# Kernel optimization log

Measured on AMD Instinct MI355X. Metric: run time of the kernel, lower is better.

Reference implementation:

```python
import jax, jax.numpy as jnp
import numpy as np

D = 512          # latent_dim
H = 8            # num_heads
NLAYERS = 8
DFF = 8          # fast_transformers d_ff slot receives num_heads in the repo (kept faithful)
NC = 10          # NUM_CLUSTERS
KMEANS_ITERS = 10
NJ, NF, T, BS = 25, 6, 1024, 16
NCLS, MAXA = 12, 6


def _pe(S, d):
    pos = jnp.arange(S, dtype=jnp.float32)[:, None]
    div = jnp.exp(jnp.arange(0, d, 2, dtype=jnp.float32) * (-np.log(10000.0) / d))
    pe = jnp.zeros((S, d), jnp.float32)
    pe = pe.at[:, 0::2].set(jnp.sin(pos * div))
    pe = pe.at[:, 1::2].set(jnp.cos(pos * div))
    return pe


def _ln(x, g, b, eps=1e-5):
    m = jnp.mean(x, -1, keepdims=True)
    v = jnp.var(x, -1, keepdims=True)
    return (x - m) * jax.lax.rsqrt(v + eps) * g + b


def _clustered_attn_one(q, k, v):
    # q, k, v: (L, Dh). Cluster queries (Lloyd k-means, deterministic init from
    # first NC queries), attend with centroids, broadcast back to queries.
    cent = q[:NC]
    for _ in range(KMEANS_ITERS):
        d = jnp.sum(cent * cent, -1)[None, :] - 2.0 * (q @ cent.T)  # (L, C)
        a = jnp.argmin(d, -1)
        oh = jax.nn.one_hot(a, NC, dtype=q.dtype)                   # (L, C)
        cent = (oh.T @ q) / jnp.maximum(oh.sum(0), 1.0)[:, None]
    d = jnp.sum(cent * cent, -1)[None, :] - 2.0 * (q @ cent.T)
    a = jnp.argmin(d, -1)                                           # (L,)
    temp = 1.0 / np.sqrt(q.shape[-1])
    A = jax.nn.softmax((cent @ k.T) * temp, -1)                     # (C, L)
    return (A @ v)[a]                                               # (L, Dh)


def _layer(z, Wq, bq, Wk, bk, Wv, bv, Wo, bo, g1, c1, g2, c2, W1, b1, W2, b2):
    B, S, d = z.shape
    Dh = d // H
    q = (z @ Wq + bq).reshape(B, S, H, Dh).transpose(0, 2, 1, 3).reshape(B * H, S, Dh)
    k = (z @ Wk + bk).reshape(B, S, H, Dh).transpose(0, 2, 1, 3).reshape(B * H, S, Dh)
    v = (z @ Wv + bv).reshape(B, S, H, Dh).transpose(0, 2, 1, 3).reshape(B * H, S, Dh)
    o = jax.vmap(_clustered_attn_one)(q, k, v)
    o = o.reshape(B, H, S, Dh).transpose(0, 2, 1, 3).reshape(B, S, d)
    z = z + (o @ Wo + bo)                     # post-norm TransformerEncoderLayer
    z = _ln(z, g1, c1)
    y = jax.nn.relu(z @ W1 + b1) @ W2 + b2    # d_ff == num_heads (repo bug, kept)
    return _ln(z + y, g2, c2)


def _forward(x, muQuery, sigmaQuery, mu_w, mu_b, sig_w, sig_b, skel_w, skel_b,
             Wq, bq, Wk, bk, Wv, bv, Wo, bo, g1, c1, g2, c2, W1, b1, W2, b2, y):
    bs, nj, nf, nframes = x.shape
    h = x.transpose(3, 0, 1, 2).reshape(nframes, bs, nj * nf) @ skel_w + skel_b  # (T,B,D)
    mu_enc = muQuery[y].reshape(bs, -1) @ mu_w + mu_b          # (B, D)
    sig_enc = sigmaQuery[y].reshape(bs, -1) @ sig_w + sig_b    # (B, D)
    xseq = jnp.concatenate([mu_enc[None], sig_enc[None], h], 0)  # (S, B, D)
    S = xseq.shape[0]
    xseq = xseq + _pe(S, xseq.shape[-1])[:, None, :]
    z = xseq.transpose(1, 0, 2)  # (B, S, D): attend over the sequence axis
    for i in range(NLAYERS):
        z = _layer(z, Wq[i], bq[i], Wk[i], bk[i], Wv[i], bv[i], Wo[i], bo[i],
                   g1[i], c1[i], g2[i], c2[i], W1[i], b1[i], W2[i], b2[i])
    out = z.transpose(1, 0, 2)  # (S, B, D)
    return out[0], out[1]       # mu, logvar: (B, D) each


def setup_inputs() -> dict:
    key = jax.random.key(0)
    ks = jax.random.split(key, 20)
    s = 0.02
    return {
        "x": jax.random.normal(ks[0], (BS, NJ, NF, T), jnp.float32),
        "y": jax.random.randint(ks[1], (BS, MAXA), 0, NCLS),
        "mask": jnp.ones((BS, T), bool),
        "muQuery": jax.random.normal(ks[2], (NCLS, D), jnp.float32),
        "sigmaQuery": jax.random.normal(ks[3], (NCLS + 1, D), jnp.float32),
        "mu_w": jax.random.normal(ks[4], (D * MAXA, D), jnp.float32) * s,
        "mu_b": jnp.zeros((D,), jnp.float32),
        "sig_w": jax.random.normal(ks[5], (D * MAXA, D), jnp.float32) * s,
        "sig_b": jnp.zeros((D,), jnp.float32),
        "skel_w": jax.random.normal(ks[6], (NJ * NF, D), jnp.float32) * s,
        "skel_b": jnp.zeros((D,), jnp.float32),
        "Wq": jax.random.normal(ks[7], (NLAYERS, D, D), jnp.float32) * s,
        "bq": jnp.zeros((NLAYERS, D), jnp.float32),
        "Wk": jax.random.normal(ks[8], (NLAYERS, D, D), jnp.float32) * s,
        "bk": jnp.zeros((NLAYERS, D), jnp.float32),
        "Wv": jax.random.normal(ks[9], (NLAYERS, D, D), jnp.float32) * s,
        "bv": jnp.zeros((NLAYERS, D), jnp.float32),
        "Wo": jax.random.normal(ks[10], (NLAYERS, D, D), jnp.float32) * s,
        "bo": jnp.zeros((NLAYERS, D), jnp.float32),
        "g1": jnp.ones((NLAYERS, D), jnp.float32),
        "c1": jnp.zeros((NLAYERS, D), jnp.float32),
        "g2": jnp.ones((NLAYERS, D), jnp.float32),
        "c2": jnp.zeros((NLAYERS, D), jnp.float32),
        "W1": jax.random.normal(ks[11], (NLAYERS, D, DFF), jnp.float32) * s,
        "b1": jnp.zeros((NLAYERS, DFF), jnp.float32),
        "W2": jax.random.normal(ks[12], (NLAYERS, DFF, D), jnp.float32) * s,
        "b2": jnp.zeros((NLAYERS, D), jnp.float32),
    }


def reference(x, y, mask, muQuery, sigmaQuery, mu_w, mu_b, sig_w, sig_b,
              skel_w, skel_b, Wq, bq, Wk, bk, Wv, bv, Wo, bo,
              g1, c1, g2, c2, W1, b1, W2, b2):
    del mask  # computed but never passed to the encoder in the original code
    mu, logvar = _forward(x, muQuery, sigmaQuery, mu_w, mu_b, sig_w, sig_b,
                          skel_w, skel_b, Wq, bq, Wk, bk, Wv, bv, Wo, bo,
                          g1, c1, g2, c2, W1, b1, W2, b2, y)
    return mu, logvar
```

## Files before the change

kernel.cpp:

```cpp
#include <hip/hip_runtime.h>
#include <hip/hip_fp16.h>
#include <math.h>

#define D 512
#define H 8
#define DH 64
#define NLAYERS 8
#define DFF 8
#define NC 10
#define KITERS 10
#define SEQ 1026
#define SEQP 1032
#define BATCH 16
#define MR (BATCH*SEQ)
#define NBUF ((size_t)MR * D)
#define DD ((size_t)D * D)

typedef _Float16 f16;
typedef f16 f16x8 __attribute__((ext_vector_type(8)));
typedef float f32x4 __attribute__((ext_vector_type(4)));

__device__ __forceinline__ void split2(float x, float y, unsigned& uh, unsigned& ul) {
    __half hx = __float2half_rn(x), hy = __float2half_rn(y);
    __half lx = __float2half_rn(x - __half2float(hx));
    __half ly = __float2half_rn(y - __half2float(hy));
    uh = (unsigned)__half_as_ushort(hx) | ((unsigned)__half_as_ushort(hy) << 16);
    ul = (unsigned)__half_as_ushort(lx) | ((unsigned)__half_as_ushort(ly) << 16);
}

__device__ __forceinline__ float pe_val(int s, int d) {
    float e = (float)(d & ~1);
    float dv = expf(e * (-9.210340371976184f / 512.0f));
    float ph = (float)s * dv;
    return (d & 1) ? cosf(ph) : sinf(ph);
}

__launch_bounds__(256)
__global__ void convert_w(const float* __restrict__ Wq, const float* __restrict__ Wk,
                          const float* __restrict__ Wv, const float* __restrict__ Wo,
                          ushort* __restrict__ whiT, ushort* __restrict__ wloT)
{
    __shared__ float tile[64][65];
    const int tid = threadIdx.x;
    const int k0 = blockIdx.x * 64, n0 = blockIdx.y * 64, m = blockIdx.z;
    const float* W;
    switch (m) { case 0: W = Wq; break; case 1: W = Wk; break;
                 case 2: W = Wv; break; default: W = Wo; }
    {
        int r = tid >> 4, c = (tid & 15) * 4;
        #pragma unroll
        for (int p = 0; p < 4; ++p) {
            float4 v = *(const float4*)&W[(size_t)(k0 + r + p*16)*D + n0 + c];
            tile[r + p*16][c]   = v.x; tile[r + p*16][c+1] = v.y;
            tile[r + p*16][c+2] = v.z; tile[r + p*16][c+3] = v.w;
        }
    }
    __syncthreads();
    ushort* ohp = whiT + (size_t)m * DD;
    ushort* olp = wloT + (size_t)m * DD;
    {
        int nl = tid >> 3, kc = (tid & 7) * 8;
        #pragma unroll
        for (int p = 0; p < 2; ++p) {
            int n = nl + p*32;
            uint4 UH, UL;
            split2(tile[kc+0][n], tile[kc+1][n], UH.x, UL.x);
            split2(tile[kc+2][n], tile[kc+3][n], UH.y, UL.y);
            split2(tile[kc+4][n], tile[kc+5][n], UH.z, UL.z);
            split2(tile[kc+6][n], tile[kc+7][n], UH.w, UL.w);
            size_t off = (size_t)(n0 + n)*D + k0 + kc;
            *(uint4*)&ohp[off] = UH;
            *(uint4*)&olp[off] = UL;
        }
    }
}

__launch_bounds__(256)
__global__ void embed_kernel(const float* __restrict__ x, const int* __restrict__ y,
    const float* __restrict__ muQ, const float* __restrict__ sigQ,
    const float* __restrict__ mu_w, const float* __restrict__ mu_b,
    const float* __restrict__ sig_w, const float* __restrict__ sig_b,
    const float* __restrict__ skel_w, const float* __restrict__ skel_b,
    float* __restrict__ z)
{
    __shared__ float xin[3072];
    const int bx = blockIdx.x, b = blockIdx.y, tid = threadIdx.x;
    if (bx < 2) {
        const float* Q  = (bx == 0) ? muQ  : sigQ;
        const float* W  = (bx == 0) ? mu_w : sig_w;
        const float* bb = (bx == 0) ? mu_b : sig_b;
        for (int i = tid; i < 3072; i += 256) {
            int a = y[b*6 + (i >> 9)];
            xin[i] = Q[a*D + (i & 511)];
        }
        __syncthreads();
        const int d0 = tid, d1 = tid + 256;
        float acc0 = bb[d0], acc1 = bb[d1];
        const float4* x4 = (const float4*)xin;
        for (int i4 = 0; i4 < 768; ++i4) {
            float4 xv = x4[i4];
            int r = i4 * 4;
            acc0 += xv.x*W[(size_t)(r+0)*D+d0] + xv.y*W[(size_t)(r+1)*D+d0]
                  + xv.z*W[(size_t)(r+2)*D+d0] + xv.w*W[(size_t)(r+3)*D+d0];
            acc1 += xv.x*W[(size_t)(r+0)*D+d1] + xv.y*W[(size_t)(r+1)*D+d1]
                  + xv.z*W[(size_t)(r+2)*D+d1] + xv.w*W[(size_t)(r+3)*D+d1];
        }
        size_t base = ((size_t)b*SEQ + bx) * D;
        z[base + d0] = acc0 + pe_val(bx, d0);
        z[base + d1] = acc1 + pe_val(bx, d1);
    } else {
        const int f0 = (bx - 2) * 4;
        for (int idx = tid; idx < 600; idx += 256) {
            int i = idx >> 2, ff = idx & 3;
            xin[idx] = x[((size_t)(b*150 + i))*1024 + f0 + ff];
        }
        __syncthreads();
        const float4* x4 = (const float4*)xin;
        for (int dd = 0; dd < 2; ++dd) {
            const int d = tid + dd*256;
            float a0, a1, a2, a3;
            a0 = a1 = a2 = a3 = skel_b[d];
            for (int i = 0; i < 150; ++i) {
                float4 xv = x4[i];
                float w = skel_w[(size_t)i*D + d];
                a0 += xv.x*w; a1 += xv.y*w; a2 += xv.z*w; a3 += xv.w*w;
            }
            float a[4] = {a0, a1, a2, a3};
            #pragma unroll
            for (int ff = 0; ff < 4; ++ff) {
                int s = f0 + ff + 2;
                z[((size_t)b*SEQ + s)*D + d] = a[ff] + pe_val(s, d);
            }
        }
    }
}

template<int EPI>
__launch_bounds__(256)
__global__ void gemm_f16s(const float* __restrict__ A,
                          const ushort* __restrict__ Bhi, const ushort* __restrict__ Blo,
                          const float* __restrict__ bias, const float* __restrict__ resid,
                          float* __restrict__ out, int M)
{
    __shared__ ushort Ah[128*40], Al[128*40], Bh[128*40], Bl[128*40];
    const int tid = threadIdx.x;
    const int m0 = blockIdx.y * 128, n0 = blockIdx.x * 128;
    const int l = tid & 63, wv = tid >> 6;
    const int wr = wv >> 1, wc = wv & 1;

    f32x4 acc[4][4];
    #pragma unroll
    for (int mi = 0; mi < 4; ++mi)
        #pragma unroll
        for (int ni = 0; ni < 4; ++ni) acc[mi][ni] = (f32x4){0.f, 0.f, 0.f, 0.f};

    const int ar_s = tid >> 1, ac_s = (tid & 1) * 16;
    const bool va = (m0 + ar_s) < M;
    const int r0 = (tid*2) >> 2,   kc0 = ((tid*2) & 3) * 8;
    const int r1 = (tid*2+1) >> 2, kc1 = ((tid*2+1) & 3) * 8;
    const float4 fz = make_float4(0.f, 0.f, 0.f, 0.f);

    for (int kt = 0; kt < 16; ++kt) {
        const int kb = kt * 32;
        float4 a0 = fz, a1 = fz, a2 = fz, a3 = fz;
        if (va) {
            const float4* ap = (const float4*)&A[(size_t)(m0 + ar_s)*D + kb + ac_s];
            a0 = ap[0]; a1 = ap[1]; a2 = ap[2]; a3 = ap[3];
        }
        uint4 bh0 = *(const uint4*)&Bhi[(size_t)(n0+r0)*D + kb + kc0];
        uint4 bh1 = *(const uint4*)&Bhi[(size_t)(n0+r1)*D + kb + kc1];
        uint4 bl0 = *(const uint4*)&Blo[(size_t)(n0+r0)*D + kb + kc0];
        uint4 bl1 = *(const uint4*)&Blo[(size_t)(n0+r1)*D + kb + kc1];

        uint4 AH0, AL0, AH1, AL1;
        split2(a0.x, a0.y, AH0.x, AL0.x); split2(a0.z, a0.w, AH0.y, AL0.y);
        split2(a1.x, a1.y, AH0.z, AL0.z); split2(a1.z, a1.w, AH0.w, AL0.w);
        split2(a2.x, a2.y, AH1.x, AL1.x); split2(a2.z, a2.w, AH1.y, AL1.y);
        split2(a3.x, a3.y, AH1.z, AL1.z); split2(a3.z, a3.w, AH1.w, AL1.w);

        if (kt) __syncthreads();
        *(uint4*)&Ah[ar_s*40 + ac_s]     = AH0;
        *(uint4*)&Ah[ar_s*40 + ac_s + 8] = AH1;
        *(uint4*)&Al[ar_s*40 + ac_s]     = AL0;
        *(uint4*)&Al[ar_s*40 + ac_s + 8] = AL1;
        *(uint4*)&Bh[r0*40 + kc0] = bh0;  *(uint4*)&Bh[r1*40 + kc1] = bh1;
        *(uint4*)&Bl[r0*40 + kc0] = bl0;  *(uint4*)&Bl[r1*40 + kc1] = bl1;
        __syncthreads();

        const int ko = (l >> 4) * 8;
        f16x8 bhf[4], blf[4];
        #pragma unroll
        for (int ni = 0; ni < 4; ++ni) {
            int br = wc*64 + ni*16 + (l & 15);
            bhf[ni] = *(const f16x8*)&Bh[br*40 + ko];
            blf[ni] = *(const f16x8*)&Bl[br*40 + ko];
        }
        #pragma unroll
        for (int mi = 0; mi < 4; ++mi) {
            int ar = wr*64 + mi*16 + (l & 15);
            f16x8 ahf = *(const f16x8*)&Ah[ar*40 + ko];
            f16x8 alf = *(const f16x8*)&Al[ar*40 + ko];
            #pragma unroll
            for (int ni = 0; ni < 4; ++ni) {
                acc[mi][ni] = __builtin_amdgcn_mfma_f32_16x16x32_f16(ahf, bhf[ni], acc[mi][ni], 0, 0, 0);
                acc[mi][ni] = __builtin_amdgcn_mfma_f32_16x16x32_f16(ahf, blf[ni], acc[mi][ni], 0, 0, 0);
                acc[mi][ni] = __builtin_amdgcn_mfma_f32_16x16x32_f16(alf, bhf[ni], acc[mi][ni], 0, 0, 0);
            }
        }
    }

    const int col_base = n0 + wc*64 + (l & 15);
    const int row_base = m0 + wr*64 + ((l >> 4) << 2);
    #pragma unroll
    for (int ni = 0; ni < 4; ++ni) {
        const int col = col_base + ni*16;
        const float bv = bias[col];
        #pragma unroll
        for (int mi = 0; mi < 4; ++mi) {
            #pragma unroll
            for (int e = 0; e < 4; ++e) {
                const int row = row_base + mi*16 + e;
                if (row >= M) continue;
                float val = acc[mi][ni][e] + bv;
                if (EPI == 0) {
                    int bb = row / SEQ;
                    int ss = row - bb*SEQ;
                    int hh = col >> 6, dh = col & 63;
                    out[((size_t)(bb*H + hh)*SEQ + ss)*DH + dh] = val;
                } else {
                    size_t off = (size_t)row*D + col;
                    out[off] = val + resid[off];
                }
            }
        }
    }
}

__launch_bounds__(1024, 4)
__global__ void attn_kernel(const float* __restrict__ q, const float* __restrict__ kk,
                            const float* __restrict__ v, float* __restrict__ o)
{
    __shared__ float At[NC][SEQP];
    __shared__ float cent[NC][DH];
    __shared__ float tailrow[2][DH];
    __shared__ float cnorm[NC];
    __shared__ int   cnt[NC];
    __shared__ int   chg;
    __shared__ unsigned char assign[1028];
    __shared__ float redA[16][NC];
    __shared__ float redB[16][NC];
    __shared__ float Mc[NC];
    __shared__ float Sinv[NC];

    const int tid = threadIdx.x;
    const int wv = tid >> 6, lane = tid & 63;
    const int bh = blockIdx.x;
    const int b = bh >> 3, h = bh & 7;
    const float* qh = q  + (size_t)bh * SEQ * DH;
    const float* kh = kk + (size_t)bh * SEQ * DH;
    const float* vh = v  + (size_t)bh * SEQ * DH;
    float* oh = o + (size_t)b * SEQ * D + h * DH;
    float* part = &At[0][0];

    if (tid < NC*DH) ((float*)cent)[tid] = qh[tid];
    if (tid >= NC*DH && tid < NC*DH + 2*DH) ((float*)tailrow)[tid - NC*DH] = qh[1024*DH + (tid - NC*DH)];
    __syncthreads();

    const float4* qrow4 = (const float4*)(qh + (size_t)tid * DH);
    int prev_a = -1, prev_t = -1;

    for (int iter = 0; iter <= KITERS; ++iter) {
        if (tid < NC) {
            float sn = 0.f;
            #pragma unroll
            for (int i = 0; i < 16; ++i) {
                float4 cv = *(const float4*)&cent[tid][i*4];
                sn += cv.x*cv.x + cv.y*cv.y + cv.z*cv.z + cv.w*cv.w;
            }
            cnorm[tid] = sn;
            cnt[tid] = 0;
        }
        if (tid == 0) chg = 0;
        __syncthreads();

        int a_reg;
        {
            float acc[NC];
            #pragma unroll
            for (int c = 0; c < NC; ++c) acc[c] = 0.f;
            #pragma unroll 8
            for (int kq = 0; kq < 16; ++kq) {
                float4 qv = qrow4[kq];
                #pragma unroll
                for (int c = 0; c < NC; ++c) {
                    float4 cv = *(const float4*)&cent[c][kq*4];
                    acc[c] += qv.x*cv.x + qv.y*cv.y + qv.z*cv.z + qv.w*cv.w;
                }
            }
            int best = 0; float bd = 1e30f;
            #pragma unroll
            for (int c = 0; c < NC; ++c) {
                float dd = cnorm[c] - 2.f*acc[c];
                if (dd < bd) { bd = dd; best = c; }
            }
            a_reg = best;
            assign[tid] = (unsigned char)best;
        }
        {
            unsigned long long mm = __ballot(a_reg != prev_a);
            if (lane == 0 && mm) atomicAdd(&chg, 1);
            prev_a = a_reg;
        }
        if (iter < KITERS) {
            #pragma unroll
            for (int c = 0; c < NC; ++c) {
                unsigned long long m = __ballot(a_reg == c);
                if (lane == 0 && m) atomicAdd(&cnt[c], __popcll(m));
            }
        }
        if (tid < 2) {
            int best = 0; float bd = 1e30f;
            #pragma unroll
            for (int c = 0; c < NC; ++c) {
                float acc = 0.f;
                #pragma unroll
                for (int i = 0; i < 64; ++i) acc += tailrow[tid][i]*cent[c][i];
                float dd = cnorm[c] - 2.f*acc;
                if (dd < bd) { bd = dd; best = c; }
            }
            assign[1024 + tid] = (unsigned char)best;
            if (best != prev_t) atomicAdd(&chg, 1);
            prev_t = best;
            if (iter < KITERS) atomicAdd(&cnt[best], 1);
        }
        __syncthreads();
        if (iter == KITERS) break;
        if (chg == 0) break;

        {
            float accq[NC];
            #pragma unroll
            for (int c = 0; c < NC; ++c) accq[c] = 0.f;
            const int s0 = wv * 64;
            #pragma unroll 8
            for (int i = 0; i < 64; ++i) {
                int s = s0 + i;
                float qv = qh[(size_t)s*DH + lane];
                int c = assign[s];
                #pragma unroll
                for (int cc = 0; cc < NC; ++cc) accq[cc] += (cc == c) ? qv : 0.f;
            }
            if (wv < 2) {
                int c = assign[1024 + wv];
                float qv = tailrow[wv][lane];
                #pragma unroll
                for (int cc = 0; cc < NC; ++cc) accq[cc] += (cc == c) ? qv : 0.f;
            }
            #pragma unroll
            for (int c = 0; c < NC; ++c) part[(wv*NC + c)*DH + lane] = accq[c];
        }
        __syncthreads();
        if (tid < NC*DH) {
            int c = tid >> 6;
            float s = 0.f;
            #pragma unroll
            for (int w = 0; w < 16; ++w) s += part[w*(NC*DH) + tid];
            ((float*)cent)[tid] = s / fmaxf((float)cnt[c], 1.f);
        }
        __syncthreads();
    }

    if (tid < 2*DH) ((float*)tailrow)[tid] = kh[1024*DH + tid];
    __syncthreads();

    float lg[NC], lgt[NC];
    {
        const float4* krow4 = (const float4*)(kh + (size_t)tid * DH);
        #pragma unroll
        for (int c = 0; c < NC; ++c) lg[c] = 0.f;
        #pragma unroll 8
        for (int kq = 0; kq < 16; ++kq) {
            float4 kv = krow4[kq];
            #pragma unroll
            for (int c = 0; c < NC; ++c) {
                float4 cv = *(const float4*)&cent[c][kq*4];
                lg[c] += kv.x*cv.x + kv.y*cv.y + kv.z*cv.z + kv.w*cv.w;
            }
        }
        #pragma unroll
        for (int c = 0; c < NC; ++c) lg[c] *= 0.125f;
    }
    if (tid < 2) {
        #pragma unroll
        for (int c = 0; c < NC; ++c) {
            float acc = 0.f;
            #pragma unroll
            for (int i = 0; i < 64; ++i) acc += tailrow[tid][i]*cent[c][i];
            lgt[c] = 0.125f * acc;
        }
    }

    #pragma unroll
    for (int c = 0; c < NC; ++c) {
        float m = lg[c];
        if (tid < 2) m = fmaxf(m, lgt[c]);
        #pragma unroll
        for (int off = 32; off; off >>= 1) m = fmaxf(m, __shfl_xor(m, off, 64));
        if (lane == 0) redA[wv][c] = m;
    }
    __syncthreads();
    if (tid < NC) {
        float m = redA[0][tid];
        #pragma unroll
        for (int w = 1; w < 16; ++w) m = fmaxf(m, redA[w][tid]);
        Mc[tid] = m;
    }
    __syncthreads();
    #pragma unroll
    for (int c = 0; c < NC; ++c) lg[c] = expf(lg[c] - Mc[c]);
    if (tid < 2) {
        #pragma unroll
        for (int c = 0; c < NC; ++c) lgt[c] = expf(lgt[c] - Mc[c]);
    }
    #pragma unroll
    for (int c = 0; c < NC; ++c) {
        float s = lg[c] + ((tid < 2) ? lgt[c] : 0.f);
        #pragma unroll
        for (int off = 32; off; off >>= 1) s += __shfl_xor(s, off, 64);
        if (lane == 0) redB[wv][c] = s;
    }
    __syncthreads();
    if (tid < NC) {
        float s = 0.f;
        #pragma unroll
        for (int w = 0; w < 16; ++w) s += redB[w][tid];
        Sinv[tid] = 1.f / s;
    }
    __syncthreads();
    #pragma unroll
    for (int c = 0; c < NC; ++c) At[c][tid] = lg[c] * Sinv[c];
    if (tid < 2) {
        #pragma unroll
        for (int c = 0; c < NC; ++c) At[c][1024 + tid] = lgt[c] * Sinv[c];
    }
    __syncthreads();

    {
        float accv[NC];
        #pragma unroll
        for (int c = 0; c < NC; ++c) accv[c] = 0.f;
        const int s0 = wv * 64;
        for (int i = 0; i < 64; i += 4) {
            float vv0 = vh[(size_t)(s0+i  )*DH + lane];
            float vv1 = vh[(size_t)(s0+i+1)*DH + lane];
            float vv2 = vh[(size_t)(s0+i+2)*DH + lane];
            float vv3 = vh[(size_t)(s0+i+3)*DH + lane];
            #pragma unroll
            for (int c = 0; c < NC; ++c) {
                float4 av = *(const float4*)&At[c][s0+i];
                accv[c] += av.x*vv0 + av.y*vv1 + av.z*vv2 + av.w*vv3;
            }
        }
        if (wv < 2) {
            int s = 1024 + wv;
            float vv = vh[(size_t)s*DH + lane];
            #pragma unroll
            for (int c = 0; c < NC; ++c) accv[c] += At[c][s] * vv;
        }
        __syncthreads();
        #pragma unroll
        for (int c = 0; c < NC; ++c) part[(wv*NC + c)*DH + lane] = accv[c];
    }
    __syncthreads();
    if (tid < NC*DH) {
        float s = 0.f;
        #pragma unroll
        for (int w = 0; w < 16; ++w) s += part[w*(NC*DH) + tid];
        ((float*)cent)[tid] = s;
    }
    __syncthreads();

    {
        const int s0 = wv * 64;
        #pragma unroll 4
        for (int i = 0; i < 64; ++i) {
            int s = s0 + i;
            oh[(size_t)s*D + lane] = cent[assign[s]][lane];
        }
        if (wv < 2) {
            int s = 1024 + wv;
            oh[(size_t)s*D + lane] = cent[assign[s]][lane];
        }
    }
}

__launch_bounds__(256)
__global__ void ffn_ln_kernel(const float* __restrict__ in, float* __restrict__ z,
    const float* __restrict__ g1, const float* __restrict__ c1,
    const float* __restrict__ W1, const float* __restrict__ b1,
    const float* __restrict__ W2, const float* __restrict__ b2,
    const float* __restrict__ g2, const float* __restrict__ c2)
{
    __shared__ float red[8];
    __shared__ float redh[4][DFF];
    const int row = blockIdx.x, tid = threadIdx.x;
    const int lane = tid & 63, wid = tid >> 6;
    const float* r = in + (size_t)row * D;
    float x0 = r[tid], x1 = r[tid + 256];
    float s = x0 + x1, ss = x0*x0 + x1*x1;
    #pragma unroll
    for (int off = 32; off; off >>= 1) {
        s  += __shfl_xor(s,  off, 64);
        ss += __shfl_xor(ss, off, 64);
    }
    if (lane == 0) { red[wid] = s; red[4 + wid] = ss; }
    __syncthreads();
    float tot  = red[0] + red[1] + red[2] + red[3];
    float tot2 = red[4] + red[5] + red[6] + red[7];
    float mean = tot * (1.f/512.f);
    float var  = tot2 * (1.f/512.f) - mean*mean;
    float rstd = rsqrtf(var + 1e-5f);
    float za = (x0 - mean)*rstd*g1[tid]       + c1[tid];
    float zb = (x1 - mean)*rstd*g1[tid + 256] + c1[tid + 256];

    float p[DFF];
    #pragma unroll
    for (int j = 0; j < DFF; ++j)
        p[j] = za * W1[(size_t)tid*DFF + j] + zb * W1[(size_t)(tid+256)*DFF + j];
    #pragma unroll
    for (int off = 32; off; off >>= 1)
        #pragma unroll
        for (int j = 0; j < DFF; ++j) p[j] += __shfl_xor(p[j], off, 64);
    if (lane == 0) {
        #pragma unroll
        for (int j = 0; j < DFF; ++j) redh[wid][j] = p[j];
    }
    __syncthreads();
    float hv[DFF];
    #pragma unroll
    for (int j = 0; j < DFF; ++j)
        hv[j] = fmaxf(redh[0][j] + redh[1][j] + redh[2][j] + redh[3][j] + b1[j], 0.f);
    float y0 = b2[tid], y1 = b2[tid + 256];
    #pragma unroll
    for (int j = 0; j < DFF; ++j) {
        y0 += hv[j] * W2[(size_t)j*D + tid];
        y1 += hv[j] * W2[(size_t)j*D + tid + 256];
    }
    float t0 = za + y0, t1 = zb + y1;
    float s2 = t0 + t1, ss2 = t0*t0 + t1*t1;
    #pragma unroll
    for (int off = 32; off; off >>= 1) {
        s2  += __shfl_xor(s2,  off, 64);
        ss2 += __shfl_xor(ss2, off, 64);
    }
    if (lane == 0) { red[wid] = s2; red[4 + wid] = ss2; }
    __syncthreads();
    float tt  = red[0] + red[1] + red[2] + red[3];
    float tt2 = red[4] + red[5] + red[6] + red[7];
    float m2 = tt * (1.f/512.f);
    float v2 = tt2 * (1.f/512.f) - m2*m2;
    float rstd2 = rsqrtf(v2 + 1e-5f);
    float* zo = z + (size_t)row * D;
    zo[tid]       = (t0 - m2)*rstd2*g2[tid]       + c2[tid];
    zo[tid + 256] = (t1 - m2)*rstd2*g2[tid + 256] + c2[tid + 256];
}

__launch_bounds__(256)
__global__ void extract_kernel(const float* __restrict__ z, float* __restrict__ out) {
    int i = blockIdx.x * 256 + threadIdx.x;
    if (i >= 2*BATCH*D) return;
    int half = i >> 13;
    int j = i & 8191;
    int b = j >> 9, d = j & 511;
    out[i] = z[((size_t)b*SEQ + half)*D + d];
}

extern "C" void kernel_launch(void* const* d_in, const int* in_sizes, int n_in,
                              void* d_out, int out_size, void* d_ws, size_t ws_size,
                              hipStream_t stream)
{
    const float* x      = (const float*)d_in[0];
    const int*   y      = (const int*)  d_in[1];
    const float* muQ    = (const float*)d_in[3];
    const float* sigQ   = (const float*)d_in[4];
    const float* mu_w   = (const float*)d_in[5];
    const float* mu_b   = (const float*)d_in[6];
    const float* sig_w  = (const float*)d_in[7];
    const float* sig_b  = (const float*)d_in[8];
    const float* skel_w = (const float*)d_in[9];
    const float* skel_b = (const float*)d_in[10];
    const float* Wq     = (const float*)d_in[11];
    const float* bq     = (const float*)d_in[12];
    const float* Wk     = (const float*)d_in[13];
    const float* bk     = (const float*)d_in[14];
    const float* Wv     = (const float*)d_in[15];
    const float* bv     = (const float*)d_in[16];
    const float* Wo     = (const float*)d_in[17];
    const float* bo     = (const float*)d_in[18];
    const float* g1     = (const float*)d_in[19];
    const float* c1     = (const float*)d_in[20];
    const float* g2     = (const float*)d_in[21];
    const float* c2     = (const float*)d_in[22];
    const float* W1     = (const float*)d_in[23];
    const float* b1     = (const float*)d_in[24];
    const float* W2     = (const float*)d_in[25];
    const float* b2     = (const float*)d_in[26];

    float*  z    = (float*)d_ws;
    float*  ob   = z  + NBUF;
    float*  qb   = ob + NBUF;
    float*  kb   = qb + NBUF;
    float*  vb   = kb + NBUF;
    ushort* wThi = (ushort*)(vb + NBUF);
    ushort* wTlo = wThi + 4*DD;

    embed_kernel<<<dim3(258, BATCH), 256, 0, stream>>>(
        x, y, muQ, sigQ, mu_w, mu_b, sig_w, sig_b, skel_w, skel_b, z);

    dim3 ggrid(4, 129);
    for (int l = 0; l < NLAYERS; ++l) {
        convert_w<<<dim3(8, 8, 4), 256, 0, stream>>>(
            Wq + l*DD, Wk + l*DD, Wv + l*DD, Wo + l*DD, wThi, wTlo);
        gemm_f16s<0><<<ggrid, 256, 0, stream>>>(z,  wThi,        wTlo,        bq + l*D, nullptr, qb, MR);
        gemm_f16s<0><<<ggrid, 256, 0, stream>>>(z,  wThi + DD,   wTlo + DD,   bk + l*D, nullptr, kb, MR);
        gemm_f16s<0><<<ggrid, 256, 0, stream>>>(z,  wThi + 2*DD, wTlo + 2*DD, bv + l*D, nullptr, vb, MR);
        attn_kernel<<<BATCH*H, 1024, 0, stream>>>(qb, kb, vb, ob);
        gemm_f16s<1><<<ggrid, 256, 0, stream>>>(ob, wThi + 3*DD, wTlo + 3*DD, bo + l*D, z, qb, MR);
        ffn_ln_kernel<<<MR, 256, 0, stream>>>(qb, z,
            g1 + (size_t)l*D, c1 + (size_t)l*D,
            W1 + (size_t)l*D*DFF, b1 + (size_t)l*DFF,
            W2 + (size_t)l*DFF*D, b2 + (size_t)l*D,
            g2 + (size_t)l*D, c2 + (size_t)l*D);
    }
    extract_kernel<<<64, 256, 0, stream>>>(z, (float*)d_out);

    (void)in_sizes; (void)n_in; (void)out_size; (void)ws_size;
}
```

Measured before the change: 4.911 ms.

## Use split-fp16 MFMA for k-means query-centroid distances; hoist weight conversion

```diff
diff --git a/kernel.cpp b/kernel.cpp
--- a/kernel.cpp
+++ b/kernel.cpp
@@ -43,9 +43,11 @@
     __shared__ float tile[64][65];
     const int tid = threadIdx.x;
     const int k0 = blockIdx.x * 64, n0 = blockIdx.y * 64, m = blockIdx.z;
-    const float* W;
-    switch (m) { case 0: W = Wq; break; case 1: W = Wk; break;
-                 case 2: W = Wv; break; default: W = Wo; }
+    const int which = m & 3, lyr = m >> 2;
+    const float* base;
+    switch (which) { case 0: base = Wq; break; case 1: base = Wk; break;
+                     case 2: base = Wv; break; default: base = Wo; }
+    const float* W = base + (size_t)lyr * DD;
     {
         int r = tid >> 4, c = (tid & 15) * 4;
         #pragma unroll
@@ -140,7 +142,8 @@
 __global__ void gemm_f16s(const float* __restrict__ A,
                           const ushort* __restrict__ Bhi, const ushort* __restrict__ Blo,
                           const float* __restrict__ bias, const float* __restrict__ resid,
-                          float* __restrict__ out, int M)
+                          float* __restrict__ out,
+                          ushort* __restrict__ shi, ushort* __restrict__ slo, int M)
 {
     __shared__ ushort Ah[128*40], Al[128*40], Bh[128*40], Bl[128*40];
     const int tid = threadIdx.x;
@@ -226,7 +229,13 @@
                     int bb = row / SEQ;
                     int ss = row - bb*SEQ;
                     int hh = col >> 6, dh = col & 63;
-                    out[((size_t)(bb*H + hh)*SEQ + ss)*DH + dh] = val;
+                    size_t off = ((size_t)(bb*H + hh)*SEQ + ss)*DH + dh;
+                    out[off] = val;
+                    if (shi) {
+                        __half hv2 = __float2half_rn(val);
+                        shi[off] = __half_as_ushort(hv2);
+                        slo[off] = __half_as_ushort(__float2half_rn(val - __half2float(hv2)));
+                    }
                 } else {
                     size_t off = (size_t)row*D + col;
                     out[off] = val + resid[off];
@@ -238,15 +247,18 @@
 
 __launch_bounds__(1024, 4)
 __global__ void attn_kernel(const float* __restrict__ q, const float* __restrict__ kk,
-                            const float* __restrict__ v, float* __restrict__ o)
+                            const float* __restrict__ v, float* __restrict__ o,
+                            const ushort* __restrict__ qhi, const ushort* __restrict__ qlo)
 {
     __shared__ float At[NC][SEQP];
     __shared__ float cent[NC][DH];
+    __shared__ ushort centh[16][72];
+    __shared__ ushort centl[16][72];
     __shared__ float tailrow[2][DH];
-    __shared__ float cnorm[NC];
+    __shared__ float cnorm16[16];
     __shared__ int   cnt[NC];
     __shared__ int   chg;
-    __shared__ unsigned char assign[1028];
+    __shared__ unsigned char assign[1040];
     __shared__ float redA[16][NC];
     __shared__ float redB[16][NC];
     __shared__ float Mc[NC];
@@ -259,79 +271,90 @@
     const float* qh = q  + (size_t)bh * SEQ * DH;
     const float* kh = kk + (size_t)bh * SEQ * DH;
     const float* vh = v  + (size_t)bh * SEQ * DH;
+    const ushort* qhb = qhi + (size_t)bh * SEQ * DH;
+    const ushort* qlb = qlo + (size_t)bh * SEQ * DH;
     float* oh = o + (size_t)b * SEQ * D + h * DH;
     float* part = &At[0][0];
 
     if (tid < NC*DH) ((float*)cent)[tid] = qh[tid];
     if (tid >= NC*DH && tid < NC*DH + 2*DH) ((float*)tailrow)[tid - NC*DH] = qh[1024*DH + (tid - NC*DH)];
-    __syncthreads();
-
-    const float4* qrow4 = (const float4*)(qh + (size_t)tid * DH);
-    int prev_a = -1, prev_t = -1;
+    for (int i = tid; i < 1040; i += 1024) assign[i] = 255;
+    for (int i = tid; i < 16*72; i += 1024) { (&centh[0][0])[i] = 0; (&centl[0][0])[i] = 0; }
+    __syncthreads();
 
     for (int iter = 0; iter <= KITERS; ++iter) {
-        if (tid < NC) {
-            float sn = 0.f;
-            #pragma unroll
-            for (int i = 0; i < 16; ++i) {
-                float4 cv = *(const float4*)&cent[tid][i*4];
-                sn += cv.x*cv.x + cv.y*cv.y + cv.z*cv.z + cv.w*cv.w;
-            }
-            cnorm[tid] = sn;
-            cnt[tid] = 0;
+        if (tid < 16) {
+            float sn = 1e30f;
+            if (tid < NC) {
+                sn = 0.f;
+                #pragma unroll
+                for (int i = 0; i < 16; ++i) {
+                    float4 cv = *(const float4*)&cent[tid][i*4];
+                    sn += cv.x*cv.x + cv.y*cv.y + cv.z*cv.z + cv.w*cv.w;
+                }
+                cnt[tid] = 0;
+            }
+            cnorm16[tid] = sn;
+        }
+        if (tid < 640) {
+            int c = tid >> 6, d = tid & 63;
+            float vv = cent[c][d];
+            __half hh = __float2half_rn(vv);
+            centh[c][d] = __half_as_ushort(hh);
+            centl[c][d] = __half_as_ushort(__float2half_rn(vv - __half2float(hh)));
         }
         if (tid == 0) chg = 0;
         __syncthreads();
 
-        int a_reg;
         {
-            float acc[NC];
-            #pragma unroll
-            for (int c = 0; c < NC; ++c) acc[c] = 0.f;
-            #pragma unroll 8
-            for (int kq = 0; kq < 16; ++kq) {
-                float4 qv = qrow4[kq];
-                #pragma unroll
-                for (int c = 0; c < NC; ++c) {
-                    float4 cv = *(const float4*)&cent[c][kq*4];
-                    acc[c] += qv.x*cv.x + qv.y*cv.y + qv.z*cv.z + qv.w*cv.w;
+            const int bc = lane & 15, kg = lane >> 4;
+            f16x8 B_h0 = *(const f16x8*)&centh[bc][kg*8];
+            f16x8 B_l0 = *(const f16x8*)&centl[bc][kg*8];
+            f16x8 B_h1 = *(const f16x8*)&centh[bc][32 + kg*8];
+            f16x8 B_l1 = *(const f16x8*)&centl[bc][32 + kg*8];
+            const float cn = cnorm16[bc];
+            const int ntiles = (wv == 15) ? 5 : 4;
+            for (int t = 0; t < ntiles; ++t) {
+                const int s0 = (wv*4 + t) * 16;
+                const ushort* ah = qhb + (size_t)(s0 + bc)*DH + kg*8;
+                const ushort* al = qlb + (size_t)(s0 + bc)*DH + kg*8;
+                f16x8 A_h0 = *(const f16x8*)ah;
+                f16x8 A_l0 = *(const f16x8*)al;
+                f16x8 A_h1 = *(const f16x8*)(ah + 32);
+                f16x8 A_l1 = *(const f16x8*)(al + 32);
+                f32x4 acc = (f32x4){0.f, 0.f, 0.f, 0.f};
+                acc = __builtin_amdgcn_mfma_f32_16x16x32_f16(A_h0, B_h0, acc, 0, 0, 0);
+                acc = __builtin_amdgcn_mfma_f32_16x16x32_f16(A_l0, B_h0, acc, 0, 0, 0);
+                acc = __builtin_amdgcn_mfma_f32_16x16x32_f16(A_h0, B_l0, acc, 0, 0, 0);
+                acc = __builtin_amdgcn_mfma_f32_16x16x32_f16(A_h1, B_h1, acc, 0, 0, 0);
+                acc = __builtin_amdgcn_mfma_f32_16x16x32_f16(A_l1, B_h1, acc, 0, 0, 0);
+                acc = __builtin_amdgcn_mfma_f32_16x16x32_f16(A_h1, B_l1, acc, 0, 0, 0);
+                int w0, w1, w2, w3;
+#define ARGMIN_E(EIDX, WOUT) { \
+                float dv = cn - 2.f*acc[EIDX]; int cv = bc; \
+                _Pragma("unroll") \
+                for (int off = 1; off < 16; off <<= 1) { \
+                    float d2 = __shfl_xor(dv, off, 64); \
+                    int   c2 = __shfl_xor(cv, off, 64); \
+                    if (d2 < dv || (d2 == dv && c2 < cv)) { dv = d2; cv = c2; } \
+                } \
+                WOUT = cv; }
+                ARGMIN_E(0, w0) ARGMIN_E(1, w1) ARGMIN_E(2, w2) ARGMIN_E(3, w3)
+#undef ARGMIN_E
+                if (bc == 0) {
+                    const int sb = s0 + kg*4;
+                    #pragma unroll
+                    for (int e = 0; e < 4; ++e) {
+                        int s = sb + e;
+                        if (s < SEQ) {
+                            int nw = (e == 0) ? w0 : (e == 1) ? w1 : (e == 2) ? w2 : w3;
+                            if ((int)assign[s] != nw) atomicAdd(&chg, 1);
+                            assign[s] = (unsigned char)nw;
+                            atomicAdd(&cnt[nw], 1);
+                        }
+                    }
                 }
             }
-            int best = 0; float bd = 1e30f;
-            #pragma unroll
-            for (int c = 0; c < NC; ++c) {
-                float dd = cnorm[c] - 2.f*acc[c];
-                if (dd < bd) { bd = dd; best = c; }
-            }
-            a_reg = best;
-            assign[tid] = (unsigned char)best;
-        }
-        {
-            unsigned long long mm = __ballot(a_reg != prev_a);
-            if (lane == 0 && mm) atomicAdd(&chg, 1);
-            prev_a = a_reg;
-        }
-        if (iter < KITERS) {
-            #pragma unroll
-            for (int c = 0; c < NC; ++c) {
-                unsigned long long m = __ballot(a_reg == c);
-                if (lane == 0 && m) atomicAdd(&cnt[c], __popcll(m));
-            }
-        }
-        if (tid < 2) {
-            int best = 0; float bd = 1e30f;
-            #pragma unroll
-            for (int c = 0; c < NC; ++c) {
-                float acc = 0.f;
-                #pragma unroll
-                for (int i = 0; i < 64; ++i) acc += tailrow[tid][i]*cent[c][i];
-                float dd = cnorm[c] - 2.f*acc;
-                if (dd < bd) { bd = dd; best = c; }
-            }
-            assign[1024 + tid] = (unsigned char)best;
-            if (best != prev_t) atomicAdd(&chg, 1);
-            prev_t = best;
-            if (iter < KITERS) atomicAdd(&cnt[best], 1);
         }
         __syncthreads();
         if (iter == KITERS) break;
@@ -612,20 +635,23 @@
     float*  kb   = qb + NBUF;
     float*  vb   = kb + NBUF;
     ushort* wThi = (ushort*)(vb + NBUF);
-    ushort* wTlo = wThi + 4*DD;
+    ushort* wTlo = wThi + 32*DD;
+    ushort* qhi  = wTlo + 32*DD;
+    ushort* qlo  = qhi + NBUF + 1024;
+
+    convert_w<<<dim3(8, 8, 32), 256, 0, stream>>>(Wq, Wk, Wv, Wo, wThi, wTlo);
 
     embed_kernel<<<dim3(258, BATCH), 256, 0, stream>>>(
         x, y, muQ, sigQ, mu_w, mu_b, sig_w, sig_b, skel_w, skel_b, z);
 
     dim3 ggrid(4, 129);
     for (int l = 0; l < NLAYERS; ++l) {
-        convert_w<<<dim3(8, 8, 4), 256, 0, stream>>>(
-            Wq + l*DD, Wk + l*DD, Wv + l*DD, Wo + l*DD, wThi, wTlo);
-        gemm_f16s<0><<<ggrid, 256, 0, stream>>>(z,  wThi,        wTlo,        bq + l*D, nullptr, qb, MR);
-        gemm_f16s<0><<<ggrid, 256, 0, stream>>>(z,  wThi + DD,   wTlo + DD,   bk + l*D, nullptr, kb, MR);
-        gemm_f16s<0><<<ggrid, 256, 0, stream>>>(z,  wThi + 2*DD, wTlo + 2*DD, bv + l*D, nullptr, vb, MR);
-        attn_kernel<<<BATCH*H, 1024, 0, stream>>>(qb, kb, vb, ob);
-        gemm_f16s<1><<<ggrid, 256, 0, stream>>>(ob, wThi + 3*DD, wTlo + 3*DD, bo + l*D, z, qb, MR);
+        const size_t wo = (size_t)l * 4 * DD;
+        gemm_f16s<0><<<ggrid, 256, 0, stream>>>(z,  wThi + wo,        wTlo + wo,        bq + l*D, nullptr, qb, qhi, qlo, MR);
+        gemm_f16s<0><<<ggrid, 256, 0, stream>>>(z,  wThi + wo + DD,   wTlo + wo + DD,   bk + l*D, nullptr, kb, nullptr, nullptr, MR);
+        gemm_f16s<0><<<ggrid, 256, 0, stream>>>(z,  wThi + wo + 2*DD, wTlo + wo + 2*DD, bv + l*D, nullptr, vb, nullptr, nullptr, MR);
+        attn_kernel<<<BATCH*H, 1024, 0, stream>>>(qb, kb, vb, ob, qhi, qlo);
+        gemm_f16s<1><<<ggrid, 256, 0, stream>>>(ob, wThi + wo + 3*DD, wTlo + wo + 3*DD, bo + l*D, z, qb, nullptr, nullptr, MR);
         ffn_ln_kernel<<<MR, 256, 0, stream>>>(qb, z,
             g1 + (size_t)l*D, c1 + (size_t)l*D,
             W1 + (size_t)l*D*DFF, b1 + (size_t)l*DFF,
```

Result: slower. 5.370 ms (+9.3%).

## Project cluster centroids through Wo instead of full output GEMM; batch QKV GEMMs

Applied to the files above, without the earlier changes.

```diff
diff --git a/kernel.cpp b/kernel.cpp
--- a/kernel.cpp
+++ b/kernel.cpp
@@ -15,6 +15,7 @@
 #define MR (BATCH*SEQ)
 #define NBUF ((size_t)MR * D)
 #define DD ((size_t)D * D)
+#define NBH (BATCH*H)
 
 typedef _Float16 f16;
 typedef f16 f16x8 __attribute__((ext_vector_type(8)));
@@ -37,15 +38,17 @@
 
 __launch_bounds__(256)
 __global__ void convert_w(const float* __restrict__ Wq, const float* __restrict__ Wk,
-                          const float* __restrict__ Wv, const float* __restrict__ Wo,
+                          const float* __restrict__ Wv,
                           ushort* __restrict__ whiT, ushort* __restrict__ wloT)
 {
     __shared__ float tile[64][65];
     const int tid = threadIdx.x;
     const int k0 = blockIdx.x * 64, n0 = blockIdx.y * 64, m = blockIdx.z;
-    const float* W;
-    switch (m) { case 0: W = Wq; break; case 1: W = Wk; break;
-                 case 2: W = Wv; break; default: W = Wo; }
+    const int which = m % 3, lyr = m / 3;
+    const float* base;
+    switch (which) { case 0: base = Wq; break; case 1: base = Wk; break;
+                     default: base = Wv; }
+    const float* W = base + (size_t)lyr * DD;
     {
         int r = tid >> 4, c = (tid & 15) * 4;
         #pragma unroll
@@ -135,16 +138,21 @@
     }
 }
 
-template<int EPI>
 __launch_bounds__(256)
-__global__ void gemm_f16s(const float* __restrict__ A,
-                          const ushort* __restrict__ Bhi, const ushort* __restrict__ Blo,
-                          const float* __restrict__ bias, const float* __restrict__ resid,
-                          float* __restrict__ out, int M)
+__global__ void gemm_qkv(const float* __restrict__ A,
+                         const ushort* __restrict__ Bhi_b, const ushort* __restrict__ Blo_b,
+                         const float* __restrict__ bq, const float* __restrict__ bk,
+                         const float* __restrict__ bv,
+                         float* __restrict__ outbase, int M)
 {
     __shared__ ushort Ah[128*40], Al[128*40], Bh[128*40], Bl[128*40];
     const int tid = threadIdx.x;
     const int m0 = blockIdx.y * 128, n0 = blockIdx.x * 128;
+    const int zz = blockIdx.z;
+    const ushort* Bhi = Bhi_b + (size_t)zz * DD;
+    const ushort* Blo = Blo_b + (size_t)zz * DD;
+    const float* bias = (zz == 0) ? bq : (zz == 1) ? bk : bv;
+    float* out = outbase + (size_t)zz * NBUF;
     const int l = tid & 63, wv = tid >> 6;
     const int wr = wv >> 1, wc = wv & 1;
 
@@ -214,23 +222,18 @@
     #pragma unroll
     for (int ni = 0; ni < 4; ++ni) {
         const int col = col_base + ni*16;
-        const float bv = bias[col];
+        const float bv2 = bias[col];
         #pragma unroll
         for (int mi = 0; mi < 4; ++mi) {
             #pragma unroll
             for (int e = 0; e < 4; ++e) {
                 const int row = row_base + mi*16 + e;
                 if (row >= M) continue;
-                float val = acc[mi][ni][e] + bv;
-                if (EPI == 0) {
-                    int bb = row / SEQ;
-                    int ss = row - bb*SEQ;
-                    int hh = col >> 6, dh = col & 63;
-                    out[((size_t)(bb*H + hh)*SEQ + ss)*DH + dh] = val;
-                } else {
-                    size_t off = (size_t)row*D + col;
-                    out[off] = val + resid[off];
-                }
+                float val = acc[mi][ni][e] + bv2;
+                int bb = row / SEQ;
+                int ss = row - bb*SEQ;
+                int hh = col >> 6, dh = col & 63;
+                out[((size_t)(bb*H + hh)*SEQ + ss)*DH + dh] = val;
             }
         }
     }
@@ -238,7 +241,8 @@
 
 __launch_bounds__(1024, 4)
 __global__ void attn_kernel(const float* __restrict__ q, const float* __restrict__ kk,
-                            const float* __restrict__ v, float* __restrict__ o)
+                            const float* __restrict__ v,
+                            float* __restrict__ centout, unsigned char* __restrict__ assignout)
 {
     __shared__ float At[NC][SEQP];
     __shared__ float cent[NC][DH];
@@ -255,11 +259,9 @@
     const int tid = threadIdx.x;
     const int wv = tid >> 6, lane = tid & 63;
     const int bh = blockIdx.x;
-    const int b = bh >> 3, h = bh & 7;
     const float* qh = q  + (size_t)bh * SEQ * DH;
     const float* kh = kk + (size_t)bh * SEQ * DH;
     const float* vh = v  + (size_t)bh * SEQ * DH;
-    float* oh = o + (size_t)b * SEQ * D + h * DH;
     float* part = &At[0][0];
 
     if (tid < NC*DH) ((float*)cent)[tid] = qh[tid];
@@ -476,26 +478,40 @@
         float s = 0.f;
         #pragma unroll
         for (int w = 0; w < 16; ++w) s += part[w*(NC*DH) + tid];
-        ((float*)cent)[tid] = s;
-    }
-    __syncthreads();
-
-    {
-        const int s0 = wv * 64;
-        #pragma unroll 4
-        for (int i = 0; i < 64; ++i) {
-            int s = s0 + i;
-            oh[(size_t)s*D + lane] = cent[assign[s]][lane];
-        }
-        if (wv < 2) {
-            int s = 1024 + wv;
-            oh[(size_t)s*D + lane] = cent[assign[s]][lane];
-        }
-    }
+        centout[(size_t)bh*(NC*DH) + tid] = s;
+    }
+    for (int i = tid; i < SEQ; i += 1024)
+        assignout[(size_t)bh*SEQP + i] = assign[i];
 }
 
 __launch_bounds__(256)
-__global__ void ffn_ln_kernel(const float* __restrict__ in, float* __restrict__ z,
+__global__ void pproj_kernel(const float* __restrict__ centout, const float* __restrict__ Wo,
+                             float* __restrict__ P)
+{
+    __shared__ float cs[NC][DH];
+    const int tid = threadIdx.x;
+    const int bh = blockIdx.x, h = bh & 7;
+    const int n = blockIdx.y * 256 + tid;
+    for (int i = tid; i < NC*DH; i += 256) ((float*)cs)[i] = centout[(size_t)bh*(NC*DH) + i];
+    __syncthreads();
+    float acc[NC];
+    #pragma unroll
+    for (int c = 0; c < NC; ++c) acc[c] = 0.f;
+    #pragma unroll 8
+    for (int d = 0; d < DH; ++d) {
+        float wv = Wo[(size_t)(h*DH + d)*D + n];
+        #pragma unroll
+        for (int c = 0; c < NC; ++c) acc[c] += cs[c][d] * wv;
+    }
+    #pragma unroll
+    for (int c = 0; c < NC; ++c)
+        P[((size_t)bh*NC + c)*D + n] = acc[c];
+}
+
+__launch_bounds__(256)
+__global__ void ffn_ln_kernel(float* __restrict__ z,
+    const float* __restrict__ P, const unsigned char* __restrict__ assignbuf,
+    const float* __restrict__ bo,
     const float* __restrict__ g1, const float* __restrict__ c1,
     const float* __restrict__ W1, const float* __restrict__ b1,
     const float* __restrict__ W2, const float* __restrict__ b2,
@@ -505,15 +521,25 @@
     __shared__ float redh[4][DFF];
     const int row = blockIdx.x, tid = threadIdx.x;
     const int lane = tid & 63, wid = tid >> 6;
-    const float* r = in + (size_t)row * D;
-    float x0 = r[tid], x1 = r[tid + 256];
-    float s = x0 + x1, ss = x0*x0 + x1*x1;
+    const int b = row / SEQ, s = row - b*SEQ;
+
+    float x0 = z[(size_t)row*D + tid]       + bo[tid];
+    float x1 = z[(size_t)row*D + tid + 256] + bo[tid + 256];
+    #pragma unroll
+    for (int h = 0; h < H; ++h) {
+        int a = assignbuf[(size_t)(b*H + h)*SEQP + s];
+        const float* Pr = P + ((size_t)(b*H + h)*NC + a)*D;
+        x0 += Pr[tid];
+        x1 += Pr[tid + 256];
+    }
+
+    float sm = x0 + x1, ss = x0*x0 + x1*x1;
     #pragma unroll
     for (int off = 32; off; off >>= 1) {
-        s  += __shfl_xor(s,  off, 64);
+        sm += __shfl_xor(sm, off, 64);
         ss += __shfl_xor(ss, off, 64);
     }
-    if (lane == 0) { red[wid] = s; red[4 + wid] = ss; }
+    if (lane == 0) { red[wid] = sm; red[4 + wid] = ss; }
     __syncthreads();
     float tot  = red[0] + red[1] + red[2] + red[3];
     float tot2 = red[4] + red[5] + red[6] + red[7];
@@ -607,26 +633,27 @@
     const float* b2     = (const float*)d_in[26];
 
     float*  z    = (float*)d_ws;
-    float*  ob   = z  + NBUF;
-    float*  qb   = ob + NBUF;
+    float*  qb   = z  + NBUF;
     float*  kb   = qb + NBUF;
     float*  vb   = kb + NBUF;
     ushort* wThi = (ushort*)(vb + NBUF);
-    ushort* wTlo = wThi + 4*DD;
+    ushort* wTlo = wThi + 24*DD;
+    float*  centbuf = (float*)(wTlo + 24*DD);
+    float*  P       = centbuf + (size_t)NBH*NC*DH;
+    unsigned char* assignbuf = (unsigned char*)(P + (size_t)NBH*NC*D);
+
+    convert_w<<<dim3(8, 8, 24), 256, 0, stream>>>(Wq, Wk, Wv, wThi, wTlo);
 
     embed_kernel<<<dim3(258, BATCH), 256, 0, stream>>>(
         x, y, muQ, sigQ, mu_w, mu_b, sig_w, sig_b, skel_w, skel_b, z);
 
-    dim3 ggrid(4, 129);
     for (int l = 0; l < NLAYERS; ++l) {
-        convert_w<<<dim3(8, 8, 4), 256, 0, stream>>>(
-            Wq + l*DD, Wk + l*DD, Wv + l*DD, Wo + l*DD, wThi, wTlo);
-        gemm_f16s<0><<<ggrid, 256, 0, stream>>>(z,  wThi,        wTlo,        bq + l*D, nullptr, qb, MR);
-        gemm_f16s<0><<<ggrid, 256, 0, stream>>>(z,  wThi + DD,   wTlo + DD,   bk + l*D, nullptr, kb, MR);
-        gemm_f16s<0><<<ggrid, 256, 0, stream>>>(z,  wThi + 2*DD, wTlo + 2*DD, bv + l*D, nullptr, vb, MR);
-        attn_kernel<<<BATCH*H, 1024, 0, stream>>>(qb, kb, vb, ob);
-        gemm_f16s<1><<<ggrid, 256, 0, stream>>>(ob, wThi + 3*DD, wTlo + 3*DD, bo + l*D, z, qb, MR);
-        ffn_ln_kernel<<<MR, 256, 0, stream>>>(qb, z,
+        gemm_qkv<<<dim3(4, 129, 3), 256, 0, stream>>>(
+            z, wThi + (size_t)l*3*DD, wTlo + (size_t)l*3*DD,
+            bq + l*D, bk + l*D, bv + l*D, qb, MR);
+        attn_kernel<<<NBH, 1024, 0, stream>>>(qb, kb, vb, centbuf, assignbuf);
+        pproj_kernel<<<dim3(NBH, 2), 256, 0, stream>>>(centbuf, Wo + (size_t)l*DD, P);
+        ffn_ln_kernel<<<MR, 256, 0, stream>>>(z, P, assignbuf, bo + l*D,
             g1 + (size_t)l*D, c1 + (size_t)l*D,
             W1 + (size_t)l*D*DFF, b1 + (size_t)l*DFF,
             W2 + (size_t)l*DFF*D, b2 + (size_t)l*D,
```

New measurement: 4.468 ms. 9.0% less time.
